# Performance work log

Hardware: AMD Instinct MI355X
Metric: run time of the kernel (lower is better)

The kernel has to match this reference:

```python
import jax, jax.numpy as jnp
import numpy as np
from jax import lax

BN_EPS = 1e-5


def _condconv(x, w, b, fc_w, fc_b):
    """CondConv2D: per-sample expert mixing then 3x3 conv (pad=1, stride=1).
    x: [B, Cin, H, W]; w: [E, Cout, Cin, 3, 3]; b: [Cout]; fc_w: [E, Cin]; fc_b: [E].
    """
    B, Cin, H, W = x.shape
    E, Cout, _, kh, kw = w.shape
    pooled = x.mean(axis=(2, 3))                               # [B, Cin] adaptive_avg_pool2d(1,1)+flatten
    rw = jax.nn.sigmoid(pooled @ fc_w.T + fc_b)                # [B, E] routing weights
    kernels = jnp.einsum('be,eoihw->boihw', rw, w)             # [B, Cout, Cin, 3, 3]
    # Batched per-sample conv via grouped conv: groups = B
    xi = x.reshape(1, B * Cin, H, W)
    ker = kernels.reshape(B * Cout, Cin, kh, kw)
    out = lax.conv_general_dilated(
        xi, ker, window_strides=(1, 1), padding=((1, 1), (1, 1)),
        feature_group_count=B,
        dimension_numbers=('NCHW', 'OIHW', 'NCHW'))
    return out.reshape(B, Cout, H, W) + b[None, :, None, None]


def _bn_relu(x, g, b, m, v):
    # eval-mode BatchNorm2d followed by ReLU
    inv = g * lax.rsqrt(v + BN_EPS)
    return jax.nn.relu(x * inv[None, :, None, None] + (b - m * inv)[None, :, None, None])


def setup_inputs() -> dict:
    key = jax.random.key(0)
    ks = jax.random.split(key, 8)
    B, Cin, Cout, H, W, E = 16, 64, 128, 128, 128, 3
    s1 = 1.0 / np.sqrt(Cin * 9)
    s2 = 1.0 / np.sqrt(Cout * 9)
    return {
        'x': jax.random.normal(ks[0], (B, Cin, H, W), jnp.float32),
        'w1': jax.random.normal(ks[1], (E, Cout, Cin, 3, 3), jnp.float32) * s1,
        'b1': jax.random.normal(ks[2], (Cout,), jnp.float32) * s1,
        'fc1_w': jax.random.normal(ks[3], (E, Cin), jnp.float32) / np.sqrt(Cin),
        'fc1_b': jnp.zeros((E,), jnp.float32),
        'bn1_g': jnp.ones((Cout,), jnp.float32),
        'bn1_b': jnp.zeros((Cout,), jnp.float32),
        'bn1_m': jnp.zeros((Cout,), jnp.float32),
        'bn1_v': jnp.ones((Cout,), jnp.float32),
        'w2': jax.random.normal(ks[4], (E, Cout, Cout, 3, 3), jnp.float32) * s2,
        'b2': jax.random.normal(ks[5], (Cout,), jnp.float32) * s2,
        'fc2_w': jax.random.normal(ks[6], (E, Cout), jnp.float32) / np.sqrt(Cout),
        'fc2_b': jnp.zeros((E,), jnp.float32),
        'bn2_g': jnp.ones((Cout,), jnp.float32),
        'bn2_b': jnp.zeros((Cout,), jnp.float32),
        'bn2_m': jnp.zeros((Cout,), jnp.float32),
        'bn2_v': jnp.ones((Cout,), jnp.float32),
    }


def reference(x, w1, b1, fc1_w, fc1_b, bn1_g, bn1_b, bn1_m, bn1_v,
              w2, b2, fc2_w, fc2_b, bn2_g, bn2_b, bn2_m, bn2_v):
    h = _condconv(x, w1, b1, fc1_w, fc1_b)
    h = _bn_relu(h, bn1_g, bn1_b, bn1_m, bn1_v)
    h = _condconv(h, w2, b2, fc2_w, fc2_b)
    h = _bn_relu(h, bn2_g, bn2_b, bn2_m, bn2_v)
    return h
```

## Files before the change

kernel.cpp:

```cpp
#include <hip/hip_runtime.h>
#include <math.h>

#define BN_EPS 1e-5f

typedef short bf16x8 __attribute__((ext_vector_type(8)));
typedef float f32x4 __attribute__((ext_vector_type(4)));
typedef float f32x16 __attribute__((ext_vector_type(16)));
typedef unsigned short ushort8v __attribute__((ext_vector_type(8)));
typedef unsigned int uint;
typedef unsigned short ushort;

__device__ inline ushort f2bf(float f) {
    uint u = __float_as_uint(f);
    uint r = u + 0x7FFFu + ((u >> 16) & 1u);
    return (ushort)(r >> 16);
}
__device__ inline float bf2f(ushort u) { return __uint_as_float(((uint)u) << 16); }
__device__ inline uint cvtpk(float lo, float hi) {
    uint r;
    asm("v_cvt_pk_bf16_f32 %0, %1, %2" : "=v"(r) : "v"(lo), "v"(hi));
    return r;
}

__global__ void scsh_kernel(const float* b1, const float* g1, const float* bb1,
                            const float* m1, const float* v1,
                            const float* b2, const float* g2, const float* bb2,
                            const float* m2, const float* v2,
                            float* scsh1, float* scsh2) {
    int t = threadIdx.x;
    if (t < 128) {
        float sc = g1[t] * rsqrtf(v1[t] + BN_EPS);
        scsh1[t] = sc;
        scsh1[128 + t] = (b1[t] - m1[t]) * sc + bb1[t];
    } else {
        int c = t - 128;
        float sc = g2[c] * rsqrtf(v2[c] + BN_EPS);
        scsh2[c] = sc;
        scsh2[128 + c] = (b2[c] - m2[c]) * sc + bb2[c];
    }
}

__global__ void xprep_kernel(const float* __restrict__ x, ushort* __restrict__ xT,
                             float* __restrict__ pooled1) {
    __shared__ float t[64][65];
    const int b = blockIdx.y;
    const int p0 = blockIdx.x * 64;
    const int tid = threadIdx.x;
#pragma unroll
    for (int it = 0; it < 16; ++it) {
        const int idx = it * 256 + tid;
        const int ci = idx >> 6, p = idx & 63;
        t[ci][p] = x[((size_t)b * 64 + ci) * 16384 + p0 + p];
    }
    __syncthreads();
    const int h = p0 >> 7;
#pragma unroll
    for (int it = 0; it < 2; ++it) {
        const int p = it * 32 + (tid >> 3);
        const int w = (p0 & 127) + p;
        const int c0 = (tid & 7) * 8;
        const int cc = c0 >> 4;
        ushort8v u;
#pragma unroll
        for (int j = 0; j < 8; ++j) u[j] = f2bf(t[c0 + j][p]);
        *(ushort8v*)&xT[(((size_t)(b * 128 + h) * 4 + cc) * 128 + w) * 16 + (c0 & 15)] = u;
    }
    if (tid < 64) {
        float s = 0.f;
#pragma unroll 8
        for (int p = 0; p < 64; ++p) s += t[tid][p];
        atomicAdd(&pooled1[b * 64 + tid], s);
    }
}

__global__ void pool2h_kernel(const ushort* __restrict__ hT, float* __restrict__ pooled2) {
    const int b = blockIdx.x, slab = blockIdx.y;
    const int tid = threadIdx.x;
    const int cc = tid >> 5, o = (tid >> 4) & 1, wb = tid & 15;
    float a[8] = {0.f, 0.f, 0.f, 0.f, 0.f, 0.f, 0.f, 0.f};
    for (int r = 0; r < 4; ++r) {
        const int h = slab * 4 + r;
        const ushort* base = hT + ((size_t)(b * 128 + h) * 8 + cc) * 2048 + o * 8;
#pragma unroll
        for (int k = 0; k < 8; ++k) {
            const ushort8v u = *(const ushort8v*)(base + (wb + k * 16) * 16);
#pragma unroll
            for (int j = 0; j < 8; ++j) a[j] += bf2f(u[j]);
        }
    }
    __shared__ float sp[16][8][17];
    const int grp0 = cc * 2 + o;
#pragma unroll
    for (int j = 0; j < 8; ++j) sp[grp0][j][wb] = a[j];
    __syncthreads();
    if (tid < 128) {
        const int grp = tid >> 3, j = tid & 7;
        float s = 0.f;
#pragma unroll
        for (int k = 0; k < 16; ++k) s += sp[grp][j][k];
        const int c = (grp >> 1) * 16 + (grp & 1) * 8 + j;
        atomicAdd(&pooled2[b * 128 + c], s);
    }
}

template <int CIN>
__global__ void mix_route_kernel(const float* __restrict__ w, const float* __restrict__ pooled,
                                 const float* __restrict__ fcw, const float* __restrict__ fcb,
                                 ushort* __restrict__ wmix) {
    constexpr int NCC = CIN / 16;
    __shared__ float rwl[48];
    const int tid = threadIdx.x;
    if (tid < 48) {
        const int bb = tid / 3, e = tid % 3;
        float d = 0.f;
        for (int c = 0; c < CIN; ++c) d += pooled[bb * CIN + c] * fcw[e * CIN + c];
        const float s = fcb[e] + d * (1.f / 16384.f);
        rwl[tid] = 1.f / (1.f + expf(-s));
    }
    __syncthreads();
    const int co = blockIdx.x;
    for (int b = 0; b < 16; ++b) {
        const float r0 = rwl[b * 3 + 0], r1 = rwl[b * 3 + 1], r2 = rwl[b * 3 + 2];
        for (int idx = tid; idx < CIN * 9; idx += 256) {
            const int ci = idx & (CIN - 1);
            const int tap = idx / CIN;
            const size_t off = ((size_t)co * CIN + ci) * 9 + tap;
            const float m = r0 * w[off]
                          + r1 * w[off + (size_t)128 * CIN * 9]
                          + r2 * w[off + (size_t)2 * 128 * CIN * 9];
            const int cc = ci >> 4, o = (ci >> 3) & 1, e = ci & 7;
            const size_t dst = ((size_t)(b * NCC + cc) * 2304
                             + tap * 256 + o * 128 + co) * 8 + e;
            wmix[dst] = f2bf(m);
        }
    }
}

template <int CIN, bool TO_BF16>
__global__ __launch_bounds__(512, 2)
void conv_mfma8_kernel(const ushort* __restrict__ xT, const ushort* __restrict__ wmix,
                       const float* __restrict__ scsh,
                       float* __restrict__ outf, ushort* __restrict__ outh) {
    constexpr int NCC = CIN / 16;
    constexpr int IBUF = 24960;
    constexpr int WOFF = 2 * IBUF;
    constexpr int WBUF = 36864;
    __shared__ __align__(16) char smem[123648];

    const int L = ((blockIdx.x & 7) << 6) | (blockIdx.x >> 3);
    const int b = L >> 5;
    const int rt = L & 31;

    const int tid = threadIdx.x;
    const int lane = tid & 63, wid = tid >> 6;
    const int wm = wid >> 2, wn = wid & 3;
    const int l31 = lane & 31, lhi = lane >> 5;

    f32x16 acc[2][4];
#pragma unroll
    for (int i = 0; i < 2; ++i)
#pragma unroll
        for (int j = 0; j < 4; ++j)
#pragma unroll
            for (int r = 0; r < 16; ++r) acc[i][j][r] = 0.f;

    const ushort* inb = xT + (size_t)b * 128 * NCC * 2048;
    const ushort* wmb = wmix + (size_t)b * NCC * 18432;

    const int ihalf = wid & 1, ioct = (wid >> 1) & 1, ir0 = wid >> 2;
    const int iv = (ihalf * 64 + lane) * 16 + ioct * 8;
    const int idst0 = (ir0 * 260 + ioct * 130 + 1 + ihalf * 64) * 16;
    const int hg0 = rt * 4 - 1 + ir0;
    const int wo0 = wid * 2048 + lane * 8;
    const int wd0 = wid * 4096 + lane * 16;
    const int weo = 16384 + wid * 512 + lane * 8;
    const int wed = (32 + wid) * 1024 + lane * 16;

    auto stage = [&](char* dI, char* dW, int cc) {
        const size_t ccI = (size_t)cc * 2048;
#pragma unroll
        for (int u = 0; u < 3; ++u) {
            const int hg = hg0 + 2 * u;
            if ((unsigned)hg < 128u) {
                const ushort* src = inb + (size_t)hg * (NCC * 2048) + ccI + iv;
                __builtin_amdgcn_global_load_lds(
                    (const __attribute__((address_space(1))) void*)src,
                    (__attribute__((address_space(3))) void*)(dI + idst0 + u * 8320),
                    16, 0, 0);
            }
        }
        const ushort* ws = wmb + (size_t)cc * 18432;
#pragma unroll
        for (int u = 0; u < 4; ++u) {
            __builtin_amdgcn_global_load_lds(
                (const __attribute__((address_space(1))) void*)(ws + wo0 + u * 512),
                (__attribute__((address_space(3))) void*)(dW + wd0 + u * 1024),
                16, 0, 0);
        }
        if (wid < 4) {
            __builtin_amdgcn_global_load_lds(
                (const __attribute__((address_space(1))) void*)(ws + weo),
                (__attribute__((address_space(3))) void*)(dW + wed),
                16, 0, 0);
        }
    };

    const int ibase = (wn * 260 + lhi * 130 + l31) * 16;
    const int wbase = (lhi * 128 + wm * 64 + l31) * 16;
    const char* pI0 = smem + ibase;
    const char* pI1 = smem + IBUF + ibase;
    const char* pW0 = smem + WOFF + wbase;
    const char* pW1 = smem + WOFF + WBUF + wbase;

    auto taps = [&](const char* ldsI, const char* ldsW) {
#pragma unroll
        for (int tap = 0; tap < 9; ++tap) {
            const int dy = tap / 3, dx = tap - dy * 3;
            bf16x8 af[2];
#pragma unroll
            for (int mf = 0; mf < 2; ++mf)
                af[mf] = *(const bf16x8*)(ldsW + (tap * 4096 + mf * 512));
#pragma unroll
            for (int nf = 0; nf < 4; ++nf) {
                const bf16x8 bv = *(const bf16x8*)(ldsI + (dy * 4160 + nf * 512 + dx * 16));
#pragma unroll
                for (int mf = 0; mf < 2; ++mf)
                    acc[mf][nf] = __builtin_amdgcn_mfma_f32_32x32x16_bf16(
                        af[mf], bv, acc[mf][nf], 0, 0, 0);
            }
        }
    };

    if (tid < 48) {
        const int bi = tid >= 24, idx = tid - bi * 24;
        const int r = idx >> 2, j = idx & 3;
        const int g = r * 260 + (j >> 1) * 130 + (j & 1) * 129;
        *(f32x4*)(smem + bi * IBUF + g * 16) = f32x4{0.f, 0.f, 0.f, 0.f};
    }
    if (rt == 0 || rt == 31) {
        const int r = (rt == 0) ? 0 : 5;
        for (int g = tid; g < 520; g += 512) {
            const int bi = g >= 260, gr = g - bi * 260;
            *(f32x4*)(smem + bi * IBUF + (r * 260 + gr) * 16) = f32x4{0.f, 0.f, 0.f, 0.f};
        }
    }

    stage(smem, smem + WOFF, 0);
    __syncthreads();

    for (int cc = 0; cc < NCC; cc += 2) {
        stage(smem + IBUF, smem + WOFF + WBUF, cc + 1);
        __builtin_amdgcn_sched_barrier(0);
        taps(pI0, pW0);
        __syncthreads();
        if (cc + 2 < NCC) stage(smem, smem + WOFF, cc + 2);
        __builtin_amdgcn_sched_barrier(0);
        taps(pI1, pW1);
        __syncthreads();
    }

    if constexpr (!TO_BF16) {
#pragma unroll
        for (int mf = 0; mf < 2; ++mf) {
            const int cob = wm * 64 + mf * 32 + 4 * lhi;
            f32x4 sc[4], sh[4];
#pragma unroll
            for (int q = 0; q < 4; ++q) {
                sc[q] = *(const f32x4*)&scsh[cob + 8 * q];
                sh[q] = *(const f32x4*)&scsh[128 + cob + 8 * q];
            }
#pragma unroll
            for (int nf = 0; nf < 4; ++nf) {
                const size_t pbase = (size_t)(rt * 4 + wn) * 128 + nf * 32 + l31;
#pragma unroll
                for (int q = 0; q < 4; ++q)
#pragma unroll
                    for (int s = 0; s < 4; ++s) {
                        float y = fmaf(acc[mf][nf][q * 4 + s], sc[q][s], sh[q][s]);
                        y = y > 0.f ? y : 0.f;
                        outf[((size_t)(b * 128 + cob + 8 * q + s)) * 16384 + pbase] = y;
                    }
            }
        }
    } else {
        ushort* sf = (ushort*)smem;
#pragma unroll
        for (int p = 0; p < 2; ++p) {
            if ((wn >> 1) == p) {
                const int lr = wn & 1;
#pragma unroll
                for (int mf = 0; mf < 2; ++mf)
#pragma unroll
                    for (int q = 0; q < 4; ++q) {
                        const int co4 = wm * 64 + mf * 32 + 8 * q + 4 * lhi;
                        const f32x4 sc = *(const f32x4*)&scsh[co4];
                        const f32x4 sh = *(const f32x4*)&scsh[128 + co4];
#pragma unroll
                        for (int nf = 0; nf < 4; ++nf) {
                            const int px = lr * 128 + nf * 32 + l31;
                            float v[4];
#pragma unroll
                            for (int s = 0; s < 4; ++s) {
                                float y = fmaf(acc[mf][nf][q * 4 + s], sc[s], sh[s]);
                                v[s] = y > 0.f ? y : 0.f;
                            }
                            uint2 pk;
                            pk.x = cvtpk(v[0], v[1]);
                            pk.y = cvtpk(v[2], v[3]);
                            *(uint2*)&sf[px * 136 + co4] = pk;
                        }
                    }
            }
            __syncthreads();
#pragma unroll
            for (int it = 0; it < 4; ++it) {
                const int id = it * 512 + tid;
                const int lr = id >> 10, cc = (id >> 7) & 7, w = id & 127;
                const uint4 v0 = *(const uint4*)&sf[(lr * 128 + w) * 136 + cc * 16];
                const uint4 v1 = *(const uint4*)&sf[(lr * 128 + w) * 136 + cc * 16 + 8];
                ushort* dst = outh + (((size_t)(b * 128 + rt * 4 + 2 * p + lr)) * 8 + cc) * 2048 + w * 16;
                *(uint4*)dst = v0;
                *(uint4*)(dst + 8) = v1;
            }
            if (p == 0) __syncthreads();
        }
    }
}

extern "C" void kernel_launch(void* const* d_in, const int* in_sizes, int n_in,
                              void* d_out, int out_size, void* d_ws, size_t ws_size,
                              hipStream_t stream) {
    const float* x     = (const float*)d_in[0];
    const float* w1    = (const float*)d_in[1];
    const float* b1    = (const float*)d_in[2];
    const float* fc1_w = (const float*)d_in[3];
    const float* fc1_b = (const float*)d_in[4];
    const float* bn1g  = (const float*)d_in[5];
    const float* bn1b  = (const float*)d_in[6];
    const float* bn1m  = (const float*)d_in[7];
    const float* bn1v  = (const float*)d_in[8];
    const float* w2    = (const float*)d_in[9];
    const float* b2    = (const float*)d_in[10];
    const float* fc2_w = (const float*)d_in[11];
    const float* fc2_b = (const float*)d_in[12];
    const float* bn2g  = (const float*)d_in[13];
    const float* bn2b  = (const float*)d_in[14];
    const float* bn2m  = (const float*)d_in[15];
    const float* bn2v  = (const float*)d_in[16];

    float* out = (float*)d_out;
    char* ws = (char*)d_ws;

    ushort* hT    = (ushort*)(ws + 0);
    ushort* xT    = (ushort*)(ws + 67108864);
    ushort* wmix1 = (ushort*)(ws + 100663296);
    ushort* wmix2 = (ushort*)(ws + 103022592);
    float*  pool1 = (float*) (ws + 107741184);
    float*  pool2 = (float*) (ws + 107745280);
    float*  scsh1 = (float*) (ws + 107753472);
    float*  scsh2 = (float*) (ws + 107754496);

    hipMemsetAsync(pool1, 0, 4096, stream);
    hipMemsetAsync(pool2, 0, 8192, stream);

    scsh_kernel<<<1, 256, 0, stream>>>(b1, bn1g, bn1b, bn1m, bn1v,
                                       b2, bn2g, bn2b, bn2m, bn2v, scsh1, scsh2);

    xprep_kernel<<<dim3(256, 16), 256, 0, stream>>>(x, xT, pool1);
    mix_route_kernel<64><<<128, 256, 0, stream>>>(w1, pool1, fc1_w, fc1_b, wmix1);
    conv_mfma8_kernel<64, true><<<512, 512, 0, stream>>>(
        xT, wmix1, scsh1, nullptr, hT);

    pool2h_kernel<<<dim3(16, 32), 256, 0, stream>>>(hT, pool2);
    mix_route_kernel<128><<<128, 256, 0, stream>>>(w2, pool2, fc2_w, fc2_b, wmix2);
    conv_mfma8_kernel<128, false><<<512, 512, 0, stream>>>(
        hT, wmix2, scsh2, out, nullptr);
}
```

Measured before the change: 201.6 us.

## Split conv tiles across 16 waves per block instead of 8

The conv kernel now launches 1024 threads per block, and each wave computes half the pixel columns, so it holds a 2x2 set of MFMA accumulators instead of 2x4. Staging loads, epilogue indexing and write-back loops are redistributed across the doubled wave count, and an explicit vmcnt wait is added before the first barrier. The aim is more waves per CU to hide LDS and MFMA latency. The cost is lower per-wave reuse of the A fragments, since weights are loaded once per two N fragments instead of four. The launch_bounds(1024,4) hint may also be unattainable with ~124KB of LDS per block.

```diff
diff --git a/kernel.cpp b/kernel.cpp
--- a/kernel.cpp
+++ b/kernel.cpp
@@ -137,8 +137,8 @@
 }
 
 template <int CIN, bool TO_BF16>
-__global__ __launch_bounds__(512, 2)
-void conv_mfma8_kernel(const ushort* __restrict__ xT, const ushort* __restrict__ wmix,
+__global__ __launch_bounds__(1024, 4)
+void conv_mfma9_kernel(const ushort* __restrict__ xT, const ushort* __restrict__ wmix,
                        const float* __restrict__ scsh,
                        float* __restrict__ outf, ushort* __restrict__ outh) {
     constexpr int NCC = CIN / 16;
@@ -153,59 +153,69 @@
 
     const int tid = threadIdx.x;
     const int lane = tid & 63, wid = tid >> 6;
-    const int wm = wid >> 2, wn = wid & 3;
+    const int wm = wid >> 3;
+    const int wn8 = wid & 7;
+    const int prow = wn8 >> 1;
+    const int pcb = (wn8 & 1) * 64;
     const int l31 = lane & 31, lhi = lane >> 5;
 
-    f32x16 acc[2][4];
+    f32x16 acc[2][2];
 #pragma unroll
     for (int i = 0; i < 2; ++i)
 #pragma unroll
-        for (int j = 0; j < 4; ++j)
+        for (int j = 0; j < 2; ++j)
 #pragma unroll
             for (int r = 0; r < 16; ++r) acc[i][j][r] = 0.f;
 
     const ushort* inb = xT + (size_t)b * 128 * NCC * 2048;
     const ushort* wmb = wmix + (size_t)b * NCC * 18432;
 
-    const int ihalf = wid & 1, ioct = (wid >> 1) & 1, ir0 = wid >> 2;
+    const int ihalf = wid & 1, ioct = (wid >> 1) & 1, ir0 = (wid & 15) >> 2;
     const int iv = (ihalf * 64 + lane) * 16 + ioct * 8;
     const int idst0 = (ir0 * 260 + ioct * 130 + 1 + ihalf * 64) * 16;
     const int hg0 = rt * 4 - 1 + ir0;
-    const int wo0 = wid * 2048 + lane * 8;
-    const int wd0 = wid * 4096 + lane * 16;
-    const int weo = 16384 + wid * 512 + lane * 8;
-    const int wed = (32 + wid) * 1024 + lane * 16;
+    const int wo0 = wid * 512 + lane * 8;
+    const int wd0 = wid * 1024 + lane * 16;
 
     auto stage = [&](char* dI, char* dW, int cc) {
         const size_t ccI = (size_t)cc * 2048;
-#pragma unroll
-        for (int u = 0; u < 3; ++u) {
-            const int hg = hg0 + 2 * u;
+        {
+            const int hg = hg0;
             if ((unsigned)hg < 128u) {
                 const ushort* src = inb + (size_t)hg * (NCC * 2048) + ccI + iv;
                 __builtin_amdgcn_global_load_lds(
                     (const __attribute__((address_space(1))) void*)src,
-                    (__attribute__((address_space(3))) void*)(dI + idst0 + u * 8320),
+                    (__attribute__((address_space(3))) void*)(dI + idst0),
                     16, 0, 0);
             }
         }
+        if (wid < 8) {
+            const int hg = hg0 + 4;
+            if ((unsigned)hg < 128u) {
+                const ushort* src = inb + (size_t)hg * (NCC * 2048) + ccI + iv;
+                __builtin_amdgcn_global_load_lds(
+                    (const __attribute__((address_space(1))) void*)src,
+                    (__attribute__((address_space(3))) void*)(dI + idst0 + 4 * 4160),
+                    16, 0, 0);
+            }
+        }
         const ushort* ws = wmb + (size_t)cc * 18432;
 #pragma unroll
-        for (int u = 0; u < 4; ++u) {
+        for (int u = 0; u < 2; ++u) {
             __builtin_amdgcn_global_load_lds(
-                (const __attribute__((address_space(1))) void*)(ws + wo0 + u * 512),
-                (__attribute__((address_space(3))) void*)(dW + wd0 + u * 1024),
+                (const __attribute__((address_space(1))) void*)(ws + wo0 + u * 8192),
+                (__attribute__((address_space(3))) void*)(dW + wd0 + u * 16384),
                 16, 0, 0);
         }
         if (wid < 4) {
             __builtin_amdgcn_global_load_lds(
-                (const __attribute__((address_space(1))) void*)(ws + weo),
-                (__attribute__((address_space(3))) void*)(dW + wed),
+                (const __attribute__((address_space(1))) void*)(ws + wo0 + 16384),
+                (__attribute__((address_space(3))) void*)(dW + wd0 + 32768),
                 16, 0, 0);
         }
     };
 
-    const int ibase = (wn * 260 + lhi * 130 + l31) * 16;
+    const int ibase = (prow * 260 + lhi * 130 + pcb + l31) * 16;
     const int wbase = (lhi * 128 + wm * 64 + l31) * 16;
     const char* pI0 = smem + ibase;
     const char* pI1 = smem + IBUF + ibase;
@@ -221,7 +231,7 @@
             for (int mf = 0; mf < 2; ++mf)
                 af[mf] = *(const bf16x8*)(ldsW + (tap * 4096 + mf * 512));
 #pragma unroll
-            for (int nf = 0; nf < 4; ++nf) {
+            for (int nf = 0; nf < 2; ++nf) {
                 const bf16x8 bv = *(const bf16x8*)(ldsI + (dy * 4160 + nf * 512 + dx * 16));
 #pragma unroll
                 for (int mf = 0; mf < 2; ++mf)
@@ -239,13 +249,14 @@
     }
     if (rt == 0 || rt == 31) {
         const int r = (rt == 0) ? 0 : 5;
-        for (int g = tid; g < 520; g += 512) {
-            const int bi = g >= 260, gr = g - bi * 260;
+        if (tid < 520) {
+            const int bi = tid >= 260, gr = tid - bi * 260;
             *(f32x4*)(smem + bi * IBUF + (r * 260 + gr) * 16) = f32x4{0.f, 0.f, 0.f, 0.f};
         }
     }
 
     stage(smem, smem + WOFF, 0);
+    asm volatile("s_waitcnt vmcnt(0)" ::: "memory");
     __syncthreads();
 
     for (int cc = 0; cc < NCC; cc += 2) {
@@ -270,8 +281,8 @@
                 sh[q] = *(const f32x4*)&scsh[128 + cob + 8 * q];
             }
 #pragma unroll
-            for (int nf = 0; nf < 4; ++nf) {
-                const size_t pbase = (size_t)(rt * 4 + wn) * 128 + nf * 32 + l31;
+            for (int nf = 0; nf < 2; ++nf) {
+                const size_t pbase = (size_t)(rt * 4 + prow) * 128 + pcb + nf * 32 + l31;
 #pragma unroll
                 for (int q = 0; q < 4; ++q)
 #pragma unroll
@@ -286,8 +297,8 @@
         ushort* sf = (ushort*)smem;
 #pragma unroll
         for (int p = 0; p < 2; ++p) {
-            if ((wn >> 1) == p) {
-                const int lr = wn & 1;
+            if ((prow >> 1) == p) {
+                const int lr = prow & 1;
 #pragma unroll
                 for (int mf = 0; mf < 2; ++mf)
 #pragma unroll
@@ -296,8 +307,8 @@
                         const f32x4 sc = *(const f32x4*)&scsh[co4];
                         const f32x4 sh = *(const f32x4*)&scsh[128 + co4];
 #pragma unroll
-                        for (int nf = 0; nf < 4; ++nf) {
-                            const int px = lr * 128 + nf * 32 + l31;
+                        for (int nf = 0; nf < 2; ++nf) {
+                            const int px = lr * 128 + pcb + nf * 32 + l31;
                             float v[4];
 #pragma unroll
                             for (int s = 0; s < 4; ++s) {
@@ -313,8 +324,8 @@
             }
             __syncthreads();
 #pragma unroll
-            for (int it = 0; it < 4; ++it) {
-                const int id = it * 512 + tid;
+            for (int it = 0; it < 2; ++it) {
+                const int id = it * 1024 + tid;
                 const int lr = id >> 10, cc = (id >> 7) & 7, w = id & 127;
                 const uint4 v0 = *(const uint4*)&sf[(lr * 128 + w) * 136 + cc * 16];
                 const uint4 v1 = *(const uint4*)&sf[(lr * 128 + w) * 136 + cc * 16 + 8];
@@ -368,11 +379,11 @@
 
     xprep_kernel<<<dim3(256, 16), 256, 0, stream>>>(x, xT, pool1);
     mix_route_kernel<64><<<128, 256, 0, stream>>>(w1, pool1, fc1_w, fc1_b, wmix1);
-    conv_mfma8_kernel<64, true><<<512, 512, 0, stream>>>(
+    conv_mfma9_kernel<64, true><<<512, 1024, 0, stream>>>(
         xT, wmix1, scsh1, nullptr, hT);
 
     pool2h_kernel<<<dim3(16, 32), 256, 0, stream>>>(hT, pool2);
     mix_route_kernel<128><<<128, 256, 0, stream>>>(w2, pool2, fc2_w, fc2_b, wmix2);
-    conv_mfma8_kernel<128, false><<<512, 512, 0, stream>>>(
+    conv_mfma9_kernel<128, false><<<512, 1024, 0, stream>>>(
         hT, wmix2, scsh2, out, nullptr);
 }
```

After: 203.5 us. Within noise of the previous version (+1.0%).

## Retile conv warps to 2 rows x 64 cols and reuse input fragments across dy

Applied to the files above, without the earlier changes.

Each wave now covers two output rows by two 32-column fragments instead of one row by four fragments. Input B-fragments for rows are held in registers and slid down across dy, so each input row fragment is loaded once per three taps, which cuts LDS reads per MFMA. The convolution body moves into a force-inlined device function with two thin kernel wrappers. The cost is more live registers for the held input fragments under the 512x2 launch bounds, which risks spills.

```diff
diff --git a/kernel.cpp b/kernel.cpp
--- a/kernel.cpp
+++ b/kernel.cpp
@@ -137,10 +137,10 @@
 }
 
 template <int CIN, bool TO_BF16>
-__global__ __launch_bounds__(512, 2)
-void conv_mfma8_kernel(const ushort* __restrict__ xT, const ushort* __restrict__ wmix,
-                       const float* __restrict__ scsh,
-                       float* __restrict__ outf, ushort* __restrict__ outh) {
+__device__ __forceinline__
+void conv_core(const ushort* __restrict__ xT, const ushort* __restrict__ wmix,
+               const float* __restrict__ scsh,
+               float* __restrict__ outf, ushort* __restrict__ outh) {
     constexpr int NCC = CIN / 16;
     constexpr int IBUF = 24960;
     constexpr int WOFF = 2 * IBUF;
@@ -153,16 +153,20 @@
 
     const int tid = threadIdx.x;
     const int lane = tid & 63, wid = tid >> 6;
-    const int wm = wid >> 2, wn = wid & 3;
+    const int wm = wid >> 2;
+    const int rp = (wid >> 1) & 1;
+    const int cb = wid & 1;
     const int l31 = lane & 31, lhi = lane >> 5;
 
-    f32x16 acc[2][4];
+    f32x16 acc[2][2][2];
 #pragma unroll
     for (int i = 0; i < 2; ++i)
 #pragma unroll
-        for (int j = 0; j < 4; ++j)
-#pragma unroll
-            for (int r = 0; r < 16; ++r) acc[i][j][r] = 0.f;
+        for (int j = 0; j < 2; ++j)
+#pragma unroll
+            for (int k = 0; k < 2; ++k)
+#pragma unroll
+                for (int r = 0; r < 16; ++r) acc[i][j][k][r] = 0.f;
 
     const ushort* inb = xT + (size_t)b * 128 * NCC * 2048;
     const ushort* wmb = wmix + (size_t)b * NCC * 18432;
@@ -205,28 +209,45 @@
         }
     };
 
-    const int ibase = (wn * 260 + lhi * 130 + l31) * 16;
+    const int ibase = (rp * 2 * 260 + lhi * 130 + cb * 64 + l31) * 16;
     const int wbase = (lhi * 128 + wm * 64 + l31) * 16;
     const char* pI0 = smem + ibase;
     const char* pI1 = smem + IBUF + ibase;
     const char* pW0 = smem + WOFF + wbase;
     const char* pW1 = smem + WOFF + WBUF + wbase;
 
-    auto taps = [&](const char* ldsI, const char* ldsW) {
-#pragma unroll
-        for (int tap = 0; tap < 9; ++tap) {
-            const int dy = tap / 3, dx = tap - dy * 3;
-            bf16x8 af[2];
-#pragma unroll
-            for (int mf = 0; mf < 2; ++mf)
-                af[mf] = *(const bf16x8*)(ldsW + (tap * 4096 + mf * 512));
-#pragma unroll
-            for (int nf = 0; nf < 4; ++nf) {
-                const bf16x8 bv = *(const bf16x8*)(ldsI + (dy * 4160 + nf * 512 + dx * 16));
-#pragma unroll
-                for (int mf = 0; mf < 2; ++mf)
-                    acc[mf][nf] = __builtin_amdgcn_mfma_f32_32x32x16_bf16(
-                        af[mf], bv, acc[mf][nf], 0, 0, 0);
+    auto taps = [&](const char* pI, const char* pW) {
+        bf16x8 A0[3][2], A1[3][2];
+#pragma unroll
+        for (int dx = 0; dx < 3; ++dx)
+#pragma unroll
+            for (int cf = 0; cf < 2; ++cf) {
+                A0[dx][cf] = *(const bf16x8*)(pI + ((0 * 260) + cf * 32 + dx) * 16);
+                A1[dx][cf] = *(const bf16x8*)(pI + ((1 * 260) + cf * 32 + dx) * 16);
+            }
+#pragma unroll
+        for (int dy = 0; dy < 3; ++dy) {
+#pragma unroll
+            for (int dx = 0; dx < 3; ++dx) {
+                const int tap = dy * 3 + dx;
+                const bf16x8 af0 = *(const bf16x8*)(pW + (tap * 256) * 16);
+                const bf16x8 af1 = *(const bf16x8*)(pW + (tap * 256 + 32) * 16);
+#pragma unroll
+                for (int cf = 0; cf < 2; ++cf) {
+                    acc[0][0][cf] = __builtin_amdgcn_mfma_f32_32x32x16_bf16(af0, A0[dx][cf], acc[0][0][cf], 0, 0, 0);
+                    acc[1][0][cf] = __builtin_amdgcn_mfma_f32_32x32x16_bf16(af1, A0[dx][cf], acc[1][0][cf], 0, 0, 0);
+                    acc[0][1][cf] = __builtin_amdgcn_mfma_f32_32x32x16_bf16(af0, A1[dx][cf], acc[0][1][cf], 0, 0, 0);
+                    acc[1][1][cf] = __builtin_amdgcn_mfma_f32_32x32x16_bf16(af1, A1[dx][cf], acc[1][1][cf], 0, 0, 0);
+                }
+            }
+            if (dy < 2) {
+#pragma unroll
+                for (int dx = 0; dx < 3; ++dx)
+#pragma unroll
+                    for (int cf = 0; cf < 2; ++cf) {
+                        A0[dx][cf] = A1[dx][cf];
+                        A1[dx][cf] = *(const bf16x8*)(pI + (((dy + 2) * 260) + cf * 32 + dx) * 16);
+                    }
             }
         }
     };
@@ -270,24 +291,26 @@
                 sh[q] = *(const f32x4*)&scsh[128 + cob + 8 * q];
             }
 #pragma unroll
-            for (int nf = 0; nf < 4; ++nf) {
-                const size_t pbase = (size_t)(rt * 4 + wn) * 128 + nf * 32 + l31;
-#pragma unroll
-                for (int q = 0; q < 4; ++q)
-#pragma unroll
-                    for (int s = 0; s < 4; ++s) {
-                        float y = fmaf(acc[mf][nf][q * 4 + s], sc[q][s], sh[q][s]);
-                        y = y > 0.f ? y : 0.f;
-                        outf[((size_t)(b * 128 + cob + 8 * q + s)) * 16384 + pbase] = y;
-                    }
-            }
+            for (int rowl = 0; rowl < 2; ++rowl)
+#pragma unroll
+                for (int cf = 0; cf < 2; ++cf) {
+                    const size_t pbase = (size_t)(rt * 4 + rp * 2 + rowl) * 128
+                                       + cb * 64 + cf * 32 + l31;
+#pragma unroll
+                    for (int q = 0; q < 4; ++q)
+#pragma unroll
+                        for (int s = 0; s < 4; ++s) {
+                            float y = fmaf(acc[mf][rowl][cf][q * 4 + s], sc[q][s], sh[q][s]);
+                            y = y > 0.f ? y : 0.f;
+                            outf[((size_t)(b * 128 + cob + 8 * q + s)) * 16384 + pbase] = y;
+                        }
+                }
         }
     } else {
         ushort* sf = (ushort*)smem;
 #pragma unroll
         for (int p = 0; p < 2; ++p) {
-            if ((wn >> 1) == p) {
-                const int lr = wn & 1;
+            if (rp == p) {
 #pragma unroll
                 for (int mf = 0; mf < 2; ++mf)
 #pragma unroll
@@ -296,19 +319,21 @@
                         const f32x4 sc = *(const f32x4*)&scsh[co4];
                         const f32x4 sh = *(const f32x4*)&scsh[128 + co4];
 #pragma unroll
-                        for (int nf = 0; nf < 4; ++nf) {
-                            const int px = lr * 128 + nf * 32 + l31;
-                            float v[4];
-#pragma unroll
-                            for (int s = 0; s < 4; ++s) {
-                                float y = fmaf(acc[mf][nf][q * 4 + s], sc[s], sh[s]);
-                                v[s] = y > 0.f ? y : 0.f;
+                        for (int rowl = 0; rowl < 2; ++rowl)
+#pragma unroll
+                            for (int cf = 0; cf < 2; ++cf) {
+                                const int px = rowl * 128 + cb * 64 + cf * 32 + l31;
+                                float v[4];
+#pragma unroll
+                                for (int s = 0; s < 4; ++s) {
+                                    float y = fmaf(acc[mf][rowl][cf][q * 4 + s], sc[s], sh[s]);
+                                    v[s] = y > 0.f ? y : 0.f;
+                                }
+                                uint2 pk;
+                                pk.x = cvtpk(v[0], v[1]);
+                                pk.y = cvtpk(v[2], v[3]);
+                                *(uint2*)&sf[px * 136 + co4] = pk;
                             }
-                            uint2 pk;
-                            pk.x = cvtpk(v[0], v[1]);
-                            pk.y = cvtpk(v[2], v[3]);
-                            *(uint2*)&sf[px * 136 + co4] = pk;
-                        }
                     }
             }
             __syncthreads();
@@ -325,6 +350,17 @@
             if (p == 0) __syncthreads();
         }
     }
+}
+
+__global__ __launch_bounds__(512, 2)
+void conv1_mfma14_kernel(const ushort* __restrict__ xT, const ushort* __restrict__ wmix,
+                         const float* __restrict__ scsh, ushort* __restrict__ outh) {
+    conv_core<64, true>(xT, wmix, scsh, nullptr, outh);
+}
+__global__ __launch_bounds__(512, 2)
+void conv2_mfma14_kernel(const ushort* __restrict__ hT, const ushort* __restrict__ wmix,
+                         const float* __restrict__ scsh, float* __restrict__ outf) {
+    conv_core<128, false>(hT, wmix, scsh, outf, nullptr);
 }
 
 extern "C" void kernel_launch(void* const* d_in, const int* in_sizes, int n_in,
@@ -368,11 +404,9 @@
 
     xprep_kernel<<<dim3(256, 16), 256, 0, stream>>>(x, xT, pool1);
     mix_route_kernel<64><<<128, 256, 0, stream>>>(w1, pool1, fc1_w, fc1_b, wmix1);
-    conv_mfma8_kernel<64, true><<<512, 512, 0, stream>>>(
-        xT, wmix1, scsh1, nullptr, hT);
+    conv1_mfma14_kernel<<<512, 512, 0, stream>>>(xT, wmix1, scsh1, hT);
 
     pool2h_kernel<<<dim3(16, 32), 256, 0, stream>>>(hT, pool2);
     mix_route_kernel<128><<<128, 256, 0, stream>>>(w2, pool2, fc2_w, fc2_b, wmix2);
-    conv_mfma8_kernel<128, false><<<512, 512, 0, stream>>>(
-        hT, wmix2, scsh2, out, nullptr);
-}
+    conv2_mfma14_kernel<<<512, 512, 0, stream>>>(hT, wmix2, scsh2, out);
+}
```

Result: no change. 200.0 us (-0.8%).
